# Kernel tuning notes

Hardware: AMD Instinct MI355X
Metric: run time of the kernel (lower is better)

The kernel has to match this reference:

```python
import jax, jax.numpy as jnp
import numpy as np


def pw_dist_sq(X, Y):
    xx = jnp.sum(X * X, axis=1)[:, None]   # [N,1]
    yy = jnp.sum(Y * Y, axis=1)[None, :]   # [1,N]
    xy = X @ Y.T                            # [N,N]
    return jnp.maximum(xx + yy - 2.0 * xy, 0.0)


def setup_inputs() -> dict:
    key = jax.random.key(0)
    k1, k2 = jax.random.split(key)
    N, D = 1024, 128
    X = jax.random.normal(k1, (N, D), dtype=jnp.float32)
    Y = jax.random.normal(k2, (N, D), dtype=jnp.float32)
    return {"X": X, "Y": Y, "h": 1}


def reference(X, Y, h):
    h = float(h)
    inv_h2 = 1.0 / (h * h)
    sq_dists = pw_dist_sq(X, Y)                       # [N,N]
    K = jnp.exp(-0.5 * inv_h2 * sq_dists)             # [N,N]
    # d_K[i,j,:] = -(X[i]-Y[j])/h^2 * K[i,j]; returned reduced over j
    diff = X[:, None, :] - Y[None, :, :]              # [N,N,D]
    d_K_sum = jnp.sum(-diff * inv_h2 * K[:, :, None], axis=1)  # [N,D]
    return K, d_K_sum
```

## Files before the change

### kernel.cpp

```cpp
#include <hip/hip_runtime.h>

#define NN 1024
#define DD 128

typedef float f32x4 __attribute__((ext_vector_type(4)));
typedef _Float16 f16x4 __attribute__((ext_vector_type(4)));
typedef _Float16 f16x8 __attribute__((ext_vector_type(8)));

__device__ __forceinline__ f16x8 cvt8(f32x4 a, f32x4 b) {
  f16x8 r;
  r[0] = (_Float16)a.x; r[1] = (_Float16)a.y; r[2] = (_Float16)a.z; r[3] = (_Float16)a.w;
  r[4] = (_Float16)b.x; r[5] = (_Float16)b.y; r[6] = (_Float16)b.z; r[7] = (_Float16)b.w;
  return r;
}

#define WS_PART 8192

__global__ __launch_bounds__(256, 2) void gk_main(const float* __restrict__ X,
                                                  const float* __restrict__ Y,
                                                  const int* __restrict__ hp,
                                                  float* __restrict__ out,
                                                  float* __restrict__ ws) {
  __shared__ __align__(16) _Float16 Ks[16][136];
  __shared__ float yys[128];
  __shared__ unsigned msc[16];
  __shared__ float Sred[16];

  const int tid  = threadIdx.x;
  const int js   = blockIdx.x;
  const int ib   = blockIdx.y;
  const int lane = tid & 63;
  const int w    = tid >> 6;
  const int g    = lane >> 4;
  const int li   = lane & 15;

  const float fh = (float)hp[0];
  const float inv_h2 = 1.0f / (fh * fh);

  if (tid < 16) { msc[tid] = 0u; Sred[tid] = 0.0f; }

  const float* Xr = X + (size_t)(ib * 16 + li) * DD;
  f32x4 xa[4][2];
  #pragma unroll
  for (int kt = 0; kt < 4; ++kt) {
    int d0 = kt * 32 + g * 8;
    xa[kt][0] = *(const f32x4*)(Xr + d0);
    xa[kt][1] = *(const f32x4*)(Xr + d0 + 4);
  }
  const int dA = w * 32 + li;
  const int dB = dA + 16;
  float bpre0[4][8], bpre1[4][8];
  #pragma unroll
  for (int kt = 0; kt < 4; ++kt) {
    const float* Yb = Y + (size_t)(js * 128 + kt * 32 + g * 8) * DD;
    #pragma unroll
    for (int e = 0; e < 8; ++e) {
      bpre0[kt][e] = Yb[e * DD + dA];
      bpre1[kt][e] = Yb[e * DD + dB];
    }
  }

  float xx = 0.f;
  #pragma unroll
  for (int kt = 0; kt < 4; ++kt)
    #pragma unroll
    for (int c = 0; c < 4; ++c)
      xx += xa[kt][0][c] * xa[kt][0][c] + xa[kt][1][c] * xa[kt][1][c];
  xx += __shfl_xor(xx, 16); xx += __shfl_xor(xx, 32);

  const float* Yr0 = Y + (size_t)(js * 128 + w * 32 + li) * DD;
  const float* Yr1 = Yr0 + 16 * DD;
  f32x4 acc0 = {0.f, 0.f, 0.f, 0.f}, acc1 = {0.f, 0.f, 0.f, 0.f};
  float yy0 = 0.f, yy1 = 0.f;
  #pragma unroll
  for (int kt = 0; kt < 4; ++kt) {
    int d0 = kt * 32 + g * 8;
    f32x4 a0 = *(const f32x4*)(Yr0 + d0), b0 = *(const f32x4*)(Yr0 + d0 + 4);
    f32x4 a1 = *(const f32x4*)(Yr1 + d0), b1 = *(const f32x4*)(Yr1 + d0 + 4);
    #pragma unroll
    for (int c = 0; c < 4; ++c) {
      yy0 += a0[c] * a0[c] + b0[c] * b0[c];
      yy1 += a1[c] * a1[c] + b1[c] * b1[c];
    }
    f16x8 bf = cvt8(xa[kt][0], xa[kt][1]);
    acc0 = __builtin_amdgcn_mfma_f32_16x16x32_f16(cvt8(a0, b0), bf, acc0, 0, 0, 0);
    acc1 = __builtin_amdgcn_mfma_f32_16x16x32_f16(cvt8(a1, b1), bf, acc1, 0, 0, 0);
  }
  yy0 += __shfl_xor(yy0, 16); yy0 += __shfl_xor(yy0, 32);
  yy1 += __shfl_xor(yy1, 16); yy1 += __shfl_xor(yy1, 32);
  if (lane < 16) { yys[w * 32 + lane] = yy0; yys[w * 32 + 16 + lane] = yy1; }
  __syncthreads();

  float K[8];
  float m = 0.f, sp = 0.f;
  #pragma unroll
  for (int t = 0; t < 2; ++t) {
    f32x4 a = t ? acc1 : acc0;
    #pragma unroll
    for (int r = 0; r < 4; ++r) {
      int jl = w * 32 + t * 16 + 4 * g + r;
      float e = fminf((a[r] - 0.5f * (xx + yys[jl])) * inv_h2, 0.0f);
      float kv = exp2f(e * 1.44269504088896341f);
      K[t * 4 + r] = kv; m = fmaxf(m, kv); sp += kv;
    }
  }
  {
    float* kb = out + (size_t)(ib * 16 + li) * NN + js * 128 + w * 32 + 4 * g;
    f32x4 k0 = { K[0], K[1], K[2], K[3] };
    f32x4 k1 = { K[4], K[5], K[6], K[7] };
    *(f32x4*)kb = k0;
    *(f32x4*)(kb + 16) = k1;
  }
  m = fmaxf(m, __shfl_xor(m, 16)); m = fmaxf(m, __shfl_xor(m, 32));
  sp += __shfl_xor(sp, 16);        sp += __shfl_xor(sp, 32);
  if (lane < 16) {
    atomicMax(&msc[li], __float_as_uint(m));
    atomicAdd(&Sred[li], sp);
  }
  __syncthreads();

  {
    unsigned ue = (msc[li] >> 23) & 0xffu;
    unsigned se = 266u - ue; if (se > 254u) se = 254u;
    float scale = __uint_as_float(se << 23);
    #pragma unroll
    for (int t = 0; t < 2; ++t) {
      f16x4 q;
      #pragma unroll
      for (int r = 0; r < 4; ++r) q[r] = (_Float16)(K[t * 4 + r] * scale);
      *(f16x4*)&Ks[li][w * 32 + t * 16 + 4 * g] = q;
    }
  }
  __syncthreads();

  f32x4 c0 = {0.f, 0.f, 0.f, 0.f}, c1 = {0.f, 0.f, 0.f, 0.f};
  #pragma unroll
  for (int kt = 0; kt < 4; ++kt) {
    f16x8 af = *(const f16x8*)&Ks[li][kt * 32 + g * 8];
    f16x8 b0, b1;
    #pragma unroll
    for (int e = 0; e < 8; ++e) {
      b0[e] = (_Float16)bpre0[kt][e];
      b1[e] = (_Float16)bpre1[kt][e];
    }
    c0 = __builtin_amdgcn_mfma_f32_16x16x32_f16(af, b0, c0, 0, 0, 0);
    c1 = __builtin_amdgcn_mfma_f32_16x16x32_f16(af, b1, c1, 0, 0, 0);
  }

  float* pb = ws + WS_PART + (size_t)js * (NN * DD) + (size_t)(ib * 16) * DD;
  #pragma unroll
  for (int r = 0; r < 4; ++r) {
    int il = 4 * g + r;
    unsigned ue2 = (msc[il] >> 23) & 0xffu;
    unsigned se2 = 266u - ue2; if (se2 > 254u) se2 = 254u;
    float invs = __uint_as_float((254u - se2) << 23);
    pb[il * DD + dA] = c0[r] * invs;
    pb[il * DD + dB] = c1[r] * invs;
  }
  if (tid < 16) ws[js * NN + ib * 16 + tid] = Sred[tid];
}

__global__ __launch_bounds__(256) void dk_reduce(const float* __restrict__ X,
                                                 const int* __restrict__ hp,
                                                 const float* __restrict__ ws,
                                                 float* __restrict__ out) {
  const int unit = blockIdx.x * 256 + threadIdx.x;
  const int i  = unit >> 5;
  const int d0 = (unit & 31) * 4;
  const float fh = (float)hp[0];
  const float inv_h2 = 1.0f / (fh * fh);

  f32x4 acc = {0.f, 0.f, 0.f, 0.f};
  float s = 0.f;
  #pragma unroll
  for (int js = 0; js < 8; ++js) {
    f32x4 p = *(const f32x4*)(ws + WS_PART + (size_t)js * (NN * DD) + (size_t)i * DD + d0);
    acc.x += p.x; acc.y += p.y; acc.z += p.z; acc.w += p.w;
    s += ws[js * NN + i];
  }
  f32x4 xv = *(const f32x4*)(X + (size_t)i * DD + d0);
  f32x4 r;
  r.x = (acc.x - s * xv.x) * inv_h2;
  r.y = (acc.y - s * xv.y) * inv_h2;
  r.z = (acc.z - s * xv.z) * inv_h2;
  r.w = (acc.w - s * xv.w) * inv_h2;
  *(f32x4*)(out + (size_t)NN * NN + (size_t)i * DD + d0) = r;
}

extern "C" void kernel_launch(void* const* d_in, const int* in_sizes, int n_in,
                              void* d_out, int out_size, void* d_ws, size_t ws_size,
                              hipStream_t stream) {
  const float* X  = (const float*)d_in[0];
  const float* Y  = (const float*)d_in[1];
  const int*   hp = (const int*)d_in[2];
  float* out = (float*)d_out;
  float* ws  = (float*)d_ws;

  hipLaunchKernelGGL(gk_main, dim3(8, 64), dim3(256), 0, stream, X, Y, hp, out, ws);
  hipLaunchKernelGGL(dk_reduce, dim3(128), dim3(256), 0, stream, X, hp, ws, out);
}
```

Baseline: 17.36 us.

## Halve j-tile to 64, stage transposed Y in swizzled LDS, double grid

Each block now covers 64 Y columns instead of 128, so the grid doubles to 16x64 blocks and occupancy rises to 4 blocks per CU. The second GEMM's B operand is now built from a transposed fp16 copy of Y staged in XOR-swizzled shared memory. This replaces the strided scalar global loads into registers, aiming to cut uncoalesced traffic and register pressure. In exchange the workspace partials double to 16 slices, so the reduce kernel reads twice as much data.

New measurement: 22.01 us. +26.8%, slower.

```diff
diff --git a/kernel.cpp b/kernel.cpp
--- a/kernel.cpp
+++ b/kernel.cpp
@@ -7,6 +7,8 @@
 typedef _Float16 f16x4 __attribute__((ext_vector_type(4)));
 typedef _Float16 f16x8 __attribute__((ext_vector_type(8)));
 
+union H2 { unsigned u; _Float16 h[2]; };
+
 __device__ __forceinline__ f16x8 cvt8(f32x4 a, f32x4 b) {
   f16x8 r;
   r[0] = (_Float16)a.x; r[1] = (_Float16)a.y; r[2] = (_Float16)a.z; r[3] = (_Float16)a.w;
@@ -14,15 +16,16 @@
   return r;
 }
 
-#define WS_PART 8192
+#define WS_PART 16384
 
-__global__ __launch_bounds__(256, 2) void gk_main(const float* __restrict__ X,
+__global__ __launch_bounds__(256, 4) void gk_main(const float* __restrict__ X,
                                                   const float* __restrict__ Y,
                                                   const int* __restrict__ hp,
                                                   float* __restrict__ out,
                                                   float* __restrict__ ws) {
-  __shared__ __align__(16) _Float16 Ks[16][136];
-  __shared__ float yys[128];
+  __shared__ __align__(16) _Float16 Yt[128 * 64];
+  __shared__ __align__(16) _Float16 Ks[16 * 64];
+  __shared__ float yys[64];
   __shared__ unsigned msc[16];
   __shared__ float Sred[16];
 
@@ -39,77 +42,68 @@
 
   if (tid < 16) { msc[tid] = 0u; Sred[tid] = 0.0f; }
 
+  #pragma unroll
+  for (int p = 0; p < 2; ++p) {
+    int u  = tid + 256 * p;
+    int jp = u >> 4, ds8 = u & 15;
+    const float* ya = Y + (size_t)(js * 64 + 2 * jp) * DD + ds8 * 8;
+    f32x4 a0 = *(const f32x4*)ya,        a1 = *(const f32x4*)(ya + 4);
+    f32x4 b0 = *(const f32x4*)(ya + DD), b1 = *(const f32x4*)(ya + DD + 4);
+    int t8 = ds8 & 7;
+    #pragma unroll
+    for (int c = 0; c < 8; ++c) {
+      H2 pk;
+      pk.h[0] = (_Float16)(c < 4 ? a0[c] : a1[c - 4]);
+      pk.h[1] = (_Float16)(c < 4 ? b0[c] : b1[c - 4]);
+      int d = ds8 * 8 + c;
+      int byte = d * 128 + ((4 * jp) ^ ((c ^ t8) << 4));
+      *(unsigned*)((char*)Yt + byte) = pk.u;
+    }
+  }
+
   const float* Xr = X + (size_t)(ib * 16 + li) * DD;
   f32x4 xa[4][2];
+  float xx = 0.f;
   #pragma unroll
   for (int kt = 0; kt < 4; ++kt) {
     int d0 = kt * 32 + g * 8;
     xa[kt][0] = *(const f32x4*)(Xr + d0);
     xa[kt][1] = *(const f32x4*)(Xr + d0 + 4);
-  }
-  const int dA = w * 32 + li;
-  const int dB = dA + 16;
-  float bpre0[4][8], bpre1[4][8];
-  #pragma unroll
-  for (int kt = 0; kt < 4; ++kt) {
-    const float* Yb = Y + (size_t)(js * 128 + kt * 32 + g * 8) * DD;
-    #pragma unroll
-    for (int e = 0; e < 8; ++e) {
-      bpre0[kt][e] = Yb[e * DD + dA];
-      bpre1[kt][e] = Yb[e * DD + dB];
-    }
-  }
-
-  float xx = 0.f;
-  #pragma unroll
-  for (int kt = 0; kt < 4; ++kt)
     #pragma unroll
     for (int c = 0; c < 4; ++c)
       xx += xa[kt][0][c] * xa[kt][0][c] + xa[kt][1][c] * xa[kt][1][c];
+  }
   xx += __shfl_xor(xx, 16); xx += __shfl_xor(xx, 32);
 
-  const float* Yr0 = Y + (size_t)(js * 128 + w * 32 + li) * DD;
-  const float* Yr1 = Yr0 + 16 * DD;
-  f32x4 acc0 = {0.f, 0.f, 0.f, 0.f}, acc1 = {0.f, 0.f, 0.f, 0.f};
-  float yy0 = 0.f, yy1 = 0.f;
+  const float* Yr = Y + (size_t)(js * 64 + w * 16 + li) * DD;
+  f32x4 acc = {0.f, 0.f, 0.f, 0.f};
+  float yy = 0.f;
   #pragma unroll
   for (int kt = 0; kt < 4; ++kt) {
     int d0 = kt * 32 + g * 8;
-    f32x4 a0 = *(const f32x4*)(Yr0 + d0), b0 = *(const f32x4*)(Yr0 + d0 + 4);
-    f32x4 a1 = *(const f32x4*)(Yr1 + d0), b1 = *(const f32x4*)(Yr1 + d0 + 4);
+    f32x4 a0 = *(const f32x4*)(Yr + d0), a1 = *(const f32x4*)(Yr + d0 + 4);
     #pragma unroll
-    for (int c = 0; c < 4; ++c) {
-      yy0 += a0[c] * a0[c] + b0[c] * b0[c];
-      yy1 += a1[c] * a1[c] + b1[c] * b1[c];
-    }
-    f16x8 bf = cvt8(xa[kt][0], xa[kt][1]);
-    acc0 = __builtin_amdgcn_mfma_f32_16x16x32_f16(cvt8(a0, b0), bf, acc0, 0, 0, 0);
-    acc1 = __builtin_amdgcn_mfma_f32_16x16x32_f16(cvt8(a1, b1), bf, acc1, 0, 0, 0);
+    for (int c = 0; c < 4; ++c) yy += a0[c] * a0[c] + a1[c] * a1[c];
+    acc = __builtin_amdgcn_mfma_f32_16x16x32_f16(cvt8(a0, a1),
+                                                 cvt8(xa[kt][0], xa[kt][1]), acc, 0, 0, 0);
   }
-  yy0 += __shfl_xor(yy0, 16); yy0 += __shfl_xor(yy0, 32);
-  yy1 += __shfl_xor(yy1, 16); yy1 += __shfl_xor(yy1, 32);
-  if (lane < 16) { yys[w * 32 + lane] = yy0; yys[w * 32 + 16 + lane] = yy1; }
+  yy += __shfl_xor(yy, 16); yy += __shfl_xor(yy, 32);
+  if (lane < 16) yys[w * 16 + lane] = yy;
   __syncthreads();
 
-  float K[8];
+  float K[4];
   float m = 0.f, sp = 0.f;
   #pragma unroll
-  for (int t = 0; t < 2; ++t) {
-    f32x4 a = t ? acc1 : acc0;
-    #pragma unroll
-    for (int r = 0; r < 4; ++r) {
-      int jl = w * 32 + t * 16 + 4 * g + r;
-      float e = fminf((a[r] - 0.5f * (xx + yys[jl])) * inv_h2, 0.0f);
-      float kv = exp2f(e * 1.44269504088896341f);
-      K[t * 4 + r] = kv; m = fmaxf(m, kv); sp += kv;
-    }
+  for (int r = 0; r < 4; ++r) {
+    int jl = w * 16 + 4 * g + r;
+    float e = fminf((acc[r] - 0.5f * (xx + yys[jl])) * inv_h2, 0.0f);
+    float kv = exp2f(e * 1.44269504088896341f);
+    K[r] = kv; m = fmaxf(m, kv); sp += kv;
   }
   {
-    float* kb = out + (size_t)(ib * 16 + li) * NN + js * 128 + w * 32 + 4 * g;
+    float* kb = out + (size_t)(ib * 16 + li) * NN + js * 64 + w * 16 + 4 * g;
     f32x4 k0 = { K[0], K[1], K[2], K[3] };
-    f32x4 k1 = { K[4], K[5], K[6], K[7] };
     *(f32x4*)kb = k0;
-    *(f32x4*)(kb + 16) = k1;
   }
   m = fmaxf(m, __shfl_xor(m, 16)); m = fmaxf(m, __shfl_xor(m, 32));
   sp += __shfl_xor(sp, 16);        sp += __shfl_xor(sp, 32);
@@ -123,26 +117,24 @@
     unsigned ue = (msc[li] >> 23) & 0xffu;
     unsigned se = 266u - ue; if (se > 254u) se = 254u;
     float scale = __uint_as_float(se << 23);
+    f16x4 q;
     #pragma unroll
-    for (int t = 0; t < 2; ++t) {
-      f16x4 q;
-      #pragma unroll
-      for (int r = 0; r < 4; ++r) q[r] = (_Float16)(K[t * 4 + r] * scale);
-      *(f16x4*)&Ks[li][w * 32 + t * 16 + 4 * g] = q;
-    }
+    for (int r = 0; r < 4; ++r) q[r] = (_Float16)(K[r] * scale);
+    int byte = li * 128 + ((32 * w + 8 * g) ^ ((li & 7) << 4));
+    *(f16x4*)((char*)Ks + byte) = q;
   }
   __syncthreads();
 
+  const int dA = w * 32 + li, dB = dA + 16;
+  const int sA = ((li & 7) ^ ((dA >> 3) & 7)) << 4;
+  const int sB = ((li & 7) ^ ((dB >> 3) & 7)) << 4;
   f32x4 c0 = {0.f, 0.f, 0.f, 0.f}, c1 = {0.f, 0.f, 0.f, 0.f};
   #pragma unroll
-  for (int kt = 0; kt < 4; ++kt) {
-    f16x8 af = *(const f16x8*)&Ks[li][kt * 32 + g * 8];
-    f16x8 b0, b1;
-    #pragma unroll
-    for (int e = 0; e < 8; ++e) {
-      b0[e] = (_Float16)bpre0[kt][e];
-      b1[e] = (_Float16)bpre1[kt][e];
-    }
+  for (int kt = 0; kt < 2; ++kt) {
+    int jb = 64 * kt + 16 * g;
+    f16x8 af = *(const f16x8*)((const char*)Ks + li * 128 + (jb ^ ((li & 7) << 4)));
+    f16x8 b0 = *(const f16x8*)((const char*)Yt + dA * 128 + (jb ^ sA));
+    f16x8 b1 = *(const f16x8*)((const char*)Yt + dB * 128 + (jb ^ sB));
     c0 = __builtin_amdgcn_mfma_f32_16x16x32_f16(af, b0, c0, 0, 0, 0);
     c1 = __builtin_amdgcn_mfma_f32_16x16x32_f16(af, b1, c1, 0, 0, 0);
   }
@@ -160,11 +152,11 @@
   if (tid < 16) ws[js * NN + ib * 16 + tid] = Sred[tid];
 }
 
-__global__ __launch_bounds__(256) void dk_reduce(const float* __restrict__ X,
+__global__ __launch_bounds__(128) void dk_reduce(const float* __restrict__ X,
                                                  const int* __restrict__ hp,
                                                  const float* __restrict__ ws,
                                                  float* __restrict__ out) {
-  const int unit = blockIdx.x * 256 + threadIdx.x;
+  const int unit = blockIdx.x * 128 + threadIdx.x;
   const int i  = unit >> 5;
   const int d0 = (unit & 31) * 4;
   const float fh = (float)hp[0];
@@ -173,7 +165,7 @@
   f32x4 acc = {0.f, 0.f, 0.f, 0.f};
   float s = 0.f;
   #pragma unroll
-  for (int js = 0; js < 8; ++js) {
+  for (int js = 0; js < 16; ++js) {
     f32x4 p = *(const f32x4*)(ws + WS_PART + (size_t)js * (NN * DD) + (size_t)i * DD + d0);
     acc.x += p.x; acc.y += p.y; acc.z += p.z; acc.w += p.w;
     s += ws[js * NN + i];
@@ -196,6 +188,6 @@
   float* out = (float*)d_out;
   float* ws  = (float*)d_ws;
 
-  hipLaunchKernelGGL(gk_main, dim3(8, 64), dim3(256), 0, stream, X, Y, hp, out, ws);
-  hipLaunchKernelGGL(dk_reduce, dim3(128), dim3(256), 0, stream, X, hp, ws, out);
+  hipLaunchKernelGGL(gk_main, dim3(16, 64), dim3(256), 0, stream, X, Y, hp, out, ws);
+  hipLaunchKernelGGL(dk_reduce, dim3(256), dim3(128), 0, stream, X, hp, ws, out);
 }
```

## Reuse Y fp16 tiles from LDS per wave for K·Y MFMA, drop block-wide scale sync

Applied to the files above, without the earlier changes.

Each wave now stages its own fp16 Y slice into LDS (transposed, packed pairs) during the first GEMM. The second GEMM (K times Y) is then done per wave with a per-wave max-based scale, which removes the strided global prefetch of Y columns and the LDS atomics and barriers for the block-wide row max and sum. Per-wave partial dK results are reduced across waves through LDS before one coalesced store, and row sums go to 32 partial slots that dk_reduce adds up. dk_reduce is relaunched with more, smaller blocks. The cost is 32 KB of LDS per block, which can limit occupancy, plus extra LDS traffic, and precision changes because each wave picks its own scale.

After: 18.93 us. 9.0% more time.

```diff
diff --git a/kernel.cpp b/kernel.cpp
--- a/kernel.cpp
+++ b/kernel.cpp
@@ -4,8 +4,9 @@
 #define DD 128
 
 typedef float f32x4 __attribute__((ext_vector_type(4)));
-typedef _Float16 f16x4 __attribute__((ext_vector_type(4)));
 typedef _Float16 f16x8 __attribute__((ext_vector_type(8)));
+
+union H2 { unsigned u; _Float16 h[2]; };
 
 __device__ __forceinline__ f16x8 cvt8(f32x4 a, f32x4 b) {
   f16x8 r;
@@ -14,17 +15,14 @@
   return r;
 }
 
-#define WS_PART 8192
+#define WS_S 32768
 
 __global__ __launch_bounds__(256, 2) void gk_main(const float* __restrict__ X,
                                                   const float* __restrict__ Y,
                                                   const int* __restrict__ hp,
                                                   float* __restrict__ out,
                                                   float* __restrict__ ws) {
-  __shared__ __align__(16) _Float16 Ks[16][136];
-  __shared__ float yys[128];
-  __shared__ unsigned msc[16];
-  __shared__ float Sred[16];
+  __shared__ __align__(16) char smem[4][8192];
 
   const int tid  = threadIdx.x;
   const int js   = blockIdx.x;
@@ -37,35 +35,21 @@
   const float fh = (float)hp[0];
   const float inv_h2 = 1.0f / (fh * fh);
 
-  if (tid < 16) { msc[tid] = 0u; Sred[tid] = 0.0f; }
+  unsigned* ytp = (unsigned*)smem[w];
+  float*    dkw = (float*)smem[w];
 
   const float* Xr = X + (size_t)(ib * 16 + li) * DD;
   f32x4 xa[4][2];
+  float xx = 0.f;
   #pragma unroll
   for (int kt = 0; kt < 4; ++kt) {
     int d0 = kt * 32 + g * 8;
     xa[kt][0] = *(const f32x4*)(Xr + d0);
     xa[kt][1] = *(const f32x4*)(Xr + d0 + 4);
-  }
-  const int dA = w * 32 + li;
-  const int dB = dA + 16;
-  float bpre0[4][8], bpre1[4][8];
-  #pragma unroll
-  for (int kt = 0; kt < 4; ++kt) {
-    const float* Yb = Y + (size_t)(js * 128 + kt * 32 + g * 8) * DD;
-    #pragma unroll
-    for (int e = 0; e < 8; ++e) {
-      bpre0[kt][e] = Yb[e * DD + dA];
-      bpre1[kt][e] = Yb[e * DD + dB];
-    }
-  }
-
-  float xx = 0.f;
-  #pragma unroll
-  for (int kt = 0; kt < 4; ++kt)
     #pragma unroll
     for (int c = 0; c < 4; ++c)
       xx += xa[kt][0][c] * xa[kt][0][c] + xa[kt][1][c] * xa[kt][1][c];
+  }
   xx += __shfl_xor(xx, 16); xx += __shfl_xor(xx, 32);
 
   const float* Yr0 = Y + (size_t)(js * 128 + w * 32 + li) * DD;
@@ -75,96 +59,115 @@
   #pragma unroll
   for (int kt = 0; kt < 4; ++kt) {
     int d0 = kt * 32 + g * 8;
-    f32x4 a0 = *(const f32x4*)(Yr0 + d0), b0 = *(const f32x4*)(Yr0 + d0 + 4);
-    f32x4 a1 = *(const f32x4*)(Yr1 + d0), b1 = *(const f32x4*)(Yr1 + d0 + 4);
+    f32x4 a0 = *(const f32x4*)(Yr0 + d0), a1 = *(const f32x4*)(Yr0 + d0 + 4);
+    f32x4 b0 = *(const f32x4*)(Yr1 + d0), b1 = *(const f32x4*)(Yr1 + d0 + 4);
     #pragma unroll
     for (int c = 0; c < 4; ++c) {
-      yy0 += a0[c] * a0[c] + b0[c] * b0[c];
-      yy1 += a1[c] * a1[c] + b1[c] * b1[c];
+      yy0 += a0[c] * a0[c] + a1[c] * a1[c];
+      yy1 += b0[c] * b0[c] + b1[c] * b1[c];
+    }
+    f16x8 af0 = cvt8(a0, a1);
+    f16x8 af1 = cvt8(b0, b1);
+    #pragma unroll
+    for (int c = 0; c < 8; ++c) {
+      H2 pk; pk.h[0] = af0[c]; pk.h[1] = af1[c];
+      ytp[(d0 + c) * 16 + li] = pk.u;
     }
     f16x8 bf = cvt8(xa[kt][0], xa[kt][1]);
-    acc0 = __builtin_amdgcn_mfma_f32_16x16x32_f16(cvt8(a0, b0), bf, acc0, 0, 0, 0);
-    acc1 = __builtin_amdgcn_mfma_f32_16x16x32_f16(cvt8(a1, b1), bf, acc1, 0, 0, 0);
+    acc0 = __builtin_amdgcn_mfma_f32_16x16x32_f16(af0, bf, acc0, 0, 0, 0);
+    acc1 = __builtin_amdgcn_mfma_f32_16x16x32_f16(af1, bf, acc1, 0, 0, 0);
   }
   yy0 += __shfl_xor(yy0, 16); yy0 += __shfl_xor(yy0, 32);
   yy1 += __shfl_xor(yy1, 16); yy1 += __shfl_xor(yy1, 32);
-  if (lane < 16) { yys[w * 32 + lane] = yy0; yys[w * 32 + 16 + lane] = yy1; }
+
+  float y0r[4], y1r[4];
+  #pragma unroll
+  for (int r = 0; r < 4; ++r) {
+    y0r[r] = __shfl(yy0, 4 * g + r);
+    y1r[r] = __shfl(yy1, 4 * g + r);
+  }
+
+  float K0[4], K1[4];
+  float m = 0.f, sp = 0.f;
+  #pragma unroll
+  for (int r = 0; r < 4; ++r) {
+    float e0 = fminf((acc0[r] - 0.5f * (xx + y0r[r])) * inv_h2, 0.0f);
+    float e1 = fminf((acc1[r] - 0.5f * (xx + y1r[r])) * inv_h2, 0.0f);
+    K0[r] = exp2f(e0 * 1.44269504088896341f);
+    K1[r] = exp2f(e1 * 1.44269504088896341f);
+    m = fmaxf(m, fmaxf(K0[r], K1[r]));
+    sp += K0[r] + K1[r];
+  }
+  {
+    float* kb = out + (size_t)(ib * 16 + li) * NN + js * 128 + w * 32;
+    f32x4 k0 = { K0[0], K0[1], K0[2], K0[3] };
+    f32x4 k1 = { K1[0], K1[1], K1[2], K1[3] };
+    *(f32x4*)(kb + 4 * g) = k0;
+    *(f32x4*)(kb + 16 + 4 * g) = k1;
+  }
+  m  = fmaxf(m, __shfl_xor(m, 16));  m  = fmaxf(m, __shfl_xor(m, 32));
+  sp += __shfl_xor(sp, 16);          sp += __shfl_xor(sp, 32);
+  if (lane < 16) ws[(size_t)(js * 4 + w) * NN + ib * 16 + lane] = sp;
+
+  unsigned ue = (__float_as_uint(m) >> 23) & 0xffu;
+  unsigned se = 266u - ue; if (se > 254u) se = 254u;
+  float scale = __uint_as_float(se << 23);
+  float invs  = __uint_as_float((254u - se) << 23);
+
+  f16x8 bq;
+  #pragma unroll
+  for (int r = 0; r < 4; ++r) {
+    bq[2 * r]     = (_Float16)(K0[r] * scale);
+    bq[2 * r + 1] = (_Float16)(K1[r] * scale);
+  }
+
+  asm volatile("" ::: "memory");
+
+  f32x4 c0 = {0,0,0,0}, c1 = {0,0,0,0}, c2 = {0,0,0,0}, c3 = {0,0,0,0};
+  f32x4 c4 = {0,0,0,0}, c5 = {0,0,0,0}, c6 = {0,0,0,0}, c7 = {0,0,0,0};
+  #pragma unroll
+  for (int dt = 0; dt < 8; ++dt) {
+    int d = dt * 16 + li;
+    f16x8 af = *(const f16x8*)((const char*)ytp + d * 64 + g * 16);
+    f32x4& cc = dt == 0 ? c0 : dt == 1 ? c1 : dt == 2 ? c2 : dt == 3 ? c3
+              : dt == 4 ? c4 : dt == 5 ? c5 : dt == 6 ? c6 : c7;
+    cc = __builtin_amdgcn_mfma_f32_16x16x32_f16(af, bq, cc, 0, 0, 0);
+  }
+
+  asm volatile("" ::: "memory");
+
+  #pragma unroll
+  for (int dt = 0; dt < 8; ++dt) {
+    f32x4 cc = dt == 0 ? c0 : dt == 1 ? c1 : dt == 2 ? c2 : dt == 3 ? c3
+             : dt == 4 ? c4 : dt == 5 ? c5 : dt == 6 ? c6 : c7;
+    f32x4 v = { cc.x * invs, cc.y * invs, cc.z * invs, cc.w * invs };
+    *(f32x4*)((char*)dkw + li * 512 + dt * 64 + g * 16) = v;
+  }
   __syncthreads();
 
-  float K[8];
-  float m = 0.f, sp = 0.f;
-  #pragma unroll
-  for (int t = 0; t < 2; ++t) {
-    f32x4 a = t ? acc1 : acc0;
-    #pragma unroll
-    for (int r = 0; r < 4; ++r) {
-      int jl = w * 32 + t * 16 + 4 * g + r;
-      float e = fminf((a[r] - 0.5f * (xx + yys[jl])) * inv_h2, 0.0f);
-      float kv = exp2f(e * 1.44269504088896341f);
-      K[t * 4 + r] = kv; m = fmaxf(m, kv); sp += kv;
+  {
+    int i = tid >> 4, s = tid & 15;
+    int off = i * 128 + s * 8;
+    f32x4 r0 = {0,0,0,0}, r1 = {0,0,0,0};
+    #pragma unroll
+    for (int w2 = 0; w2 < 4; ++w2) {
+      const float* p = (const float*)smem[w2];
+      f32x4 a = *(const f32x4*)(p + off);
+      f32x4 b = *(const f32x4*)(p + off + 4);
+      r0.x += a.x; r0.y += a.y; r0.z += a.z; r0.w += a.w;
+      r1.x += b.x; r1.y += b.y; r1.z += b.z; r1.w += b.w;
     }
-  }
-  {
-    float* kb = out + (size_t)(ib * 16 + li) * NN + js * 128 + w * 32 + 4 * g;
-    f32x4 k0 = { K[0], K[1], K[2], K[3] };
-    f32x4 k1 = { K[4], K[5], K[6], K[7] };
-    *(f32x4*)kb = k0;
-    *(f32x4*)(kb + 16) = k1;
-  }
-  m = fmaxf(m, __shfl_xor(m, 16)); m = fmaxf(m, __shfl_xor(m, 32));
-  sp += __shfl_xor(sp, 16);        sp += __shfl_xor(sp, 32);
-  if (lane < 16) {
-    atomicMax(&msc[li], __float_as_uint(m));
-    atomicAdd(&Sred[li], sp);
-  }
-  __syncthreads();
-
-  {
-    unsigned ue = (msc[li] >> 23) & 0xffu;
-    unsigned se = 266u - ue; if (se > 254u) se = 254u;
-    float scale = __uint_as_float(se << 23);
-    #pragma unroll
-    for (int t = 0; t < 2; ++t) {
-      f16x4 q;
-      #pragma unroll
-      for (int r = 0; r < 4; ++r) q[r] = (_Float16)(K[t * 4 + r] * scale);
-      *(f16x4*)&Ks[li][w * 32 + t * 16 + 4 * g] = q;
-    }
-  }
-  __syncthreads();
-
-  f32x4 c0 = {0.f, 0.f, 0.f, 0.f}, c1 = {0.f, 0.f, 0.f, 0.f};
-  #pragma unroll
-  for (int kt = 0; kt < 4; ++kt) {
-    f16x8 af = *(const f16x8*)&Ks[li][kt * 32 + g * 8];
-    f16x8 b0, b1;
-    #pragma unroll
-    for (int e = 0; e < 8; ++e) {
-      b0[e] = (_Float16)bpre0[kt][e];
-      b1[e] = (_Float16)bpre1[kt][e];
-    }
-    c0 = __builtin_amdgcn_mfma_f32_16x16x32_f16(af, b0, c0, 0, 0, 0);
-    c1 = __builtin_amdgcn_mfma_f32_16x16x32_f16(af, b1, c1, 0, 0, 0);
-  }
-
-  float* pb = ws + WS_PART + (size_t)js * (NN * DD) + (size_t)(ib * 16) * DD;
-  #pragma unroll
-  for (int r = 0; r < 4; ++r) {
-    int il = 4 * g + r;
-    unsigned ue2 = (msc[il] >> 23) & 0xffu;
-    unsigned se2 = 266u - ue2; if (se2 > 254u) se2 = 254u;
-    float invs = __uint_as_float((254u - se2) << 23);
-    pb[il * DD + dA] = c0[r] * invs;
-    pb[il * DD + dB] = c1[r] * invs;
-  }
-  if (tid < 16) ws[js * NN + ib * 16 + tid] = Sred[tid];
-}
-
-__global__ __launch_bounds__(256) void dk_reduce(const float* __restrict__ X,
+    float* pb = ws + WS_S + (size_t)js * (NN * DD) + (size_t)(ib * 16 + i) * DD + s * 8;
+    *(f32x4*)pb = r0;
+    *(f32x4*)(pb + 4) = r1;
+  }
+}
+
+__global__ __launch_bounds__(128) void dk_reduce(const float* __restrict__ X,
                                                  const int* __restrict__ hp,
                                                  const float* __restrict__ ws,
                                                  float* __restrict__ out) {
-  const int unit = blockIdx.x * 256 + threadIdx.x;
+  const int unit = blockIdx.x * 128 + threadIdx.x;
   const int i  = unit >> 5;
   const int d0 = (unit & 31) * 4;
   const float fh = (float)hp[0];
@@ -173,10 +176,11 @@
   f32x4 acc = {0.f, 0.f, 0.f, 0.f};
   float s = 0.f;
   #pragma unroll
+  for (int q = 0; q < 32; ++q) s += ws[(size_t)q * NN + i];
+  #pragma unroll
   for (int js = 0; js < 8; ++js) {
-    f32x4 p = *(const f32x4*)(ws + WS_PART + (size_t)js * (NN * DD) + (size_t)i * DD + d0);
+    f32x4 p = *(const f32x4*)(ws + WS_S + (size_t)js * (NN * DD) + (size_t)i * DD + d0);
     acc.x += p.x; acc.y += p.y; acc.z += p.z; acc.w += p.w;
-    s += ws[js * NN + i];
   }
   f32x4 xv = *(const f32x4*)(X + (size_t)i * DD + d0);
   f32x4 r;
@@ -197,5 +201,5 @@
   float* ws  = (float*)d_ws;
 
   hipLaunchKernelGGL(gk_main, dim3(8, 64), dim3(256), 0, stream, X, Y, hp, out, ws);
-  hipLaunchKernelGGL(dk_reduce, dim3(128), dim3(256), 0, stream, X, hp, ws, out);
-}
+  hipLaunchKernelGGL(dk_reduce, dim3(256), dim3(128), 0, stream, X, hp, ws, out);
+}
```
